# Performance work log

Measured on AMD Instinct MI355X. Metric: run time of the kernel, lower is better.

Reference implementation:

```python
import jax, jax.numpy as jnp
import numpy as np

B, N, C_IN, C_INTER = 32, 2048, 512, 512


def setup_inputs() -> dict:
    key = jax.random.key(0)
    ks = jax.random.split(key, 10)
    s_in = 1.0 / np.sqrt(C_IN)
    s_int = 1.0 / np.sqrt(C_INTER)
    return {
        "query": jax.random.normal(ks[0], (B, N, C_IN), jnp.float32),
        "key": jax.random.normal(ks[1], (B, N, C_IN), jnp.float32),
        "Wq": jax.random.normal(ks[2], (C_IN, C_INTER), jnp.float32) * s_in,
        "bq": jnp.zeros((C_INTER,), jnp.float32),
        "Wk": jax.random.normal(ks[3], (C_IN, C_INTER), jnp.float32) * s_in,
        "bk": jnp.zeros((C_INTER,), jnp.float32),
        "Wv": jax.random.normal(ks[4], (C_IN, C_INTER), jnp.float32) * s_in,
        "bv": jnp.zeros((C_INTER,), jnp.float32),
        "Wo": jax.random.normal(ks[5], (C_INTER, C_INTER), jnp.float32) * s_int,
        "bo": jnp.zeros((C_INTER,), jnp.float32),
    }


def reference(query, key, Wq, bq, Wk, bk, Wv, bv, Wo, bo):
    value = key  # value defaults to key in original forward
    q = jnp.einsum("bnc,cd->bnd", query, Wq) + bq   # [B,N,D]
    k = jnp.einsum("bnc,cd->bnd", key, Wk) + bk
    v = jnp.einsum("bnc,cd->bnd", value, Wv) + bv
    d = q.shape[-1]
    # non-standard scaling: divide by d (not sqrt(d))
    scores = jnp.einsum("bqd,bkd->bqk", q, k) / d    # [B,N,N]
    attn = jax.nn.softmax(scores, axis=-1)
    n_kv = attn.shape[-1]
    # second non-standard scaling: divide by number of keys
    out = jnp.einsum("bqk,bkd->bqd", attn, v) / n_kv
    return jnp.einsum("bnd,de->bne", out, Wo) + bo
```

## Files before the change

### kernel.cpp

```cpp
#include <hip/hip_runtime.h>
#include <stdint.h>

typedef unsigned short u16;
typedef __attribute__((ext_vector_type(8))) short bf16x8;
typedef __attribute__((ext_vector_type(4))) float f32x4;
typedef __attribute__((ext_vector_type(2))) unsigned int u32x2;
typedef __attribute__((ext_vector_type(4))) unsigned int u32x4;

__device__ __forceinline__ float bf2f(u16 u) {
  union { unsigned int i; float f; } v; v.i = ((unsigned int)u) << 16; return v.f;
}
__device__ __forceinline__ u16 f2bf(float f) {
  union { float f; unsigned int i; } v; v.f = f;
  unsigned int x = v.i;
  return (u16)((x + 0x7fffu + ((x >> 16) & 1u)) >> 16);
}

__device__ __forceinline__ void async16(const void* g, void* l) {
  __builtin_amdgcn_global_load_lds(
      (const __attribute__((address_space(1))) void*)g,
      (__attribute__((address_space(3))) void*)l, 16, 0, 0);
}

#define VMC6 asm volatile("s_waitcnt vmcnt(6)" ::: "memory")
#define VMC0 asm volatile("s_waitcnt vmcnt(0)" ::: "memory")
#define RAWBAR()                        \
  asm volatile("" ::: "memory");        \
  __builtin_amdgcn_s_barrier();         \
  asm volatile("" ::: "memory")

__global__ __launch_bounds__(256) void cast_f32_to_bf16(
    const float* __restrict__ x, u16* __restrict__ y, long n) {
  long i = ((long)blockIdx.x * blockDim.x + threadIdx.x) * 8;
  long stride = (long)gridDim.x * blockDim.x * 8;
  for (long j = i; j < n; j += stride) {
    float4 a = ((const float4*)(x + j))[0];
    float4 b = ((const float4*)(x + j))[1];
    u32x4 o;
    o.x = (unsigned)f2bf(a.x) | ((unsigned)f2bf(a.y) << 16);
    o.y = (unsigned)f2bf(a.z) | ((unsigned)f2bf(a.w) << 16);
    o.z = (unsigned)f2bf(b.x) | ((unsigned)f2bf(b.y) << 16);
    o.w = (unsigned)f2bf(b.z) | ((unsigned)f2bf(b.w) << 16);
    __builtin_nontemporal_store(o, (u32x4*)(y + j));
  }
}

__global__ __launch_bounds__(256) void castKT(
    const float* __restrict__ Kin, u16* __restrict__ Kb, u16* __restrict__ KbT) {
  __shared__ u16 tile[32][34];
  int t = threadIdx.x;
  long b = blockIdx.z;
  int n0 = blockIdx.x * 32, c0 = blockIdx.y * 32;
  int nr = t >> 3, c4 = (t & 7) * 4;
  float4 v = *(const float4*)(Kin + (b * 2048 + n0 + nr) * 512 + c0 + c4);
  unsigned q0 = f2bf(v.x), q1 = f2bf(v.y), q2 = f2bf(v.z), q3 = f2bf(v.w);
  u32x2 o1; o1.x = q0 | (q1 << 16); o1.y = q2 | (q3 << 16);
  __builtin_nontemporal_store(o1, (u32x2*)(Kb + (b * 2048 + n0 + nr) * 512 + c0 + c4));
  tile[nr][c4] = (u16)q0; tile[nr][c4 + 1] = (u16)q1;
  tile[nr][c4 + 2] = (u16)q2; tile[nr][c4 + 3] = (u16)q3;
  __syncthreads();
  int cr = t >> 3, n4 = (t & 7) * 4;
  unsigned r0 = tile[n4][cr], r1 = tile[n4 + 1][cr];
  unsigned r2 = tile[n4 + 2][cr], r3 = tile[n4 + 3][cr];
  u32x2 o2; o2.x = r0 | (r1 << 16); o2.y = r2 | (r3 << 16);
  __builtin_nontemporal_store(o2, (u32x2*)(KbT + (b * 512 + c0 + cr) * 2048 + n0 + n4));
}

__global__ __launch_bounds__(256) void smallGT(
    const float* __restrict__ Ai, const float* __restrict__ Bi, u16* __restrict__ C) {
  __shared__ float As[16][65], Bs[16][65];
  int t = threadIdx.x;
  int i0 = blockIdx.y * 16, j0 = blockIdx.x * 16;
  int r = t >> 4, c4 = (t & 15) * 4;
  int ty = t >> 4, tx = t & 15;
  float acc = 0.f;
  for (int d0 = 0; d0 < 512; d0 += 64) {
    float4 a = *(const float4*)(Ai + (i0 + r) * 512 + d0 + c4);
    float4 b = *(const float4*)(Bi + (j0 + r) * 512 + d0 + c4);
    __syncthreads();
    As[r][c4] = a.x; As[r][c4 + 1] = a.y; As[r][c4 + 2] = a.z; As[r][c4 + 3] = a.w;
    Bs[r][c4] = b.x; Bs[r][c4 + 1] = b.y; Bs[r][c4 + 2] = b.z; Bs[r][c4 + 3] = b.w;
    __syncthreads();
#pragma unroll
    for (int d = 0; d < 64; ++d) acc += As[ty][d] * Bs[tx][d];
  }
  C[(i0 + ty) * 512 + j0 + tx] = f2bf(acc);
}

__global__ __launch_bounds__(256) void smallW2T(
    const float* __restrict__ Wv, const float* __restrict__ Wo, u16* __restrict__ C) {
  __shared__ float Vs[16][65];
  __shared__ float Os[64][17];
  int t = threadIdx.x;
  int k0 = blockIdx.x * 16, n0 = blockIdx.y * 16;
  int r = t >> 4, c4 = (t & 15) * 4;
  int dd = t >> 2, nn4 = (t & 3) * 4;
  int ty = t >> 4, tx = t & 15;
  float acc = 0.f;
  for (int d0 = 0; d0 < 512; d0 += 64) {
    float4 a = *(const float4*)(Wv + (k0 + r) * 512 + d0 + c4);
    float4 b = *(const float4*)(Wo + (long)(d0 + dd) * 512 + n0 + nn4);
    __syncthreads();
    Vs[r][c4] = a.x; Vs[r][c4 + 1] = a.y; Vs[r][c4 + 2] = a.z; Vs[r][c4 + 3] = a.w;
    Os[dd][nn4] = b.x; Os[dd][nn4 + 1] = b.y; Os[dd][nn4 + 2] = b.z; Os[dd][nn4 + 3] = b.w;
    __syncthreads();
#pragma unroll
    for (int d = 0; d < 64; ++d) acc += Vs[tx][d] * Os[d][ty];
  }
  C[(n0 + ty) * 512 + k0 + tx] = f2bf(acc);
}

__global__ __launch_bounds__(256) void wveck(
    const float* __restrict__ Wk, const float* __restrict__ bq, float* __restrict__ wv) {
  int c = blockIdx.x, t = threadIdx.x;
  float s = 0.f;
  for (int d = t; d < 512; d += 256) s += Wk[c * 512 + d] * bq[d];
  for (int off = 32; off; off >>= 1) s += __shfl_xor(s, off);
  __shared__ float r4[4];
  if ((t & 63) == 0) r4[t >> 6] = s;
  __syncthreads();
  if (t == 0) wv[c] = (r4[0] + r4[1] + r4[2] + r4[3]) * (1.0f / 512.0f);
}

__global__ __launch_bounds__(256) void cveck(
    const float* __restrict__ Wo, const float* __restrict__ bv,
    const float* __restrict__ bo, float* __restrict__ c2) {
  int e = blockIdx.x * 256 + threadIdx.x;
  float s = 0.f;
  for (int d = 0; d < 512; ++d) s += bv[d] * Wo[d * 512 + e];
  c2[e] = s * (1.0f / 2048.0f) + bo[e];
}

__global__ __launch_bounds__(256) void betak(
    const u16* __restrict__ Kb, const float* __restrict__ wv, float* __restrict__ beta) {
  __shared__ float ws[512];
  int t = threadIdx.x, lane = t & 63, wid = t >> 6;
  ws[t] = wv[t];
  ws[t + 256] = wv[t + 256];
  __syncthreads();
  long row = (long)blockIdx.x * 4 + wid;
  bf16x8 v = *(const bf16x8*)(Kb + row * 512 + lane * 8);
  float s = 0.f;
#pragma unroll
  for (int j = 0; j < 8; ++j) s += bf2f((u16)v[j]) * ws[lane * 8 + j];
  for (int off = 32; off; off >>= 1) s += __shfl_xor(s, off);
  if (lane == 0) beta[row] = s;
}

__global__ __launch_bounds__(256) void rowred(
    const float* __restrict__ psum, float* __restrict__ rinv, int nrows) {
  int r = blockIdx.x * 256 + threadIdx.x;
  if (r >= nrows) return;
  const float* p = psum + (long)r * 32;
  float s = 0.f;
#pragma unroll
  for (int j = 0; j < 32; ++j) s += p[j];
  rinv[r] = 1.0f / s;
}

template <int MODE, int EXPO>
__global__ __launch_bounds__(256, 2) void gemm(
    const u16* __restrict__ A, const u16* __restrict__ B,
    const float* __restrict__ bias, long sBias,
    const float* __restrict__ rsc, float* __restrict__ psum,
    void* __restrict__ Cout,
    int N, int K, long sA, long sB, long sC, float scale,
    int mT, int nT, int Z, int nfast) {
  __shared__ __align__(16) char lds[3][24576];
  const int t = threadIdx.x;
  const int lane = t & 63;
  const int w = t >> 6;
  const int wm = w >> 1;
  const int wn = w & 1;

  const int wg = blockIdx.x;
  const int nb = mT * nT;
  long z; int within;
  if (Z > 1 && (Z & 7) == 0) {
    int xcd = wg & 7;
    int sub = wg >> 3;
    z = (long)(sub / nb) * 8 + xcd;
    within = sub % nb;
  } else {
    z = wg / nb;
    within = wg % nb;
  }
  int bx, by;
  if (nfast) { by = within % nT; bx = within / nT; }
  else       { bx = within % mT; by = within / mT; }
  const long m0 = (long)bx * 256;
  const int n0 = by * 128;
  const int nt = K >> 5;

  const int srow = w * 16 + (lane >> 2);
  const int koff = 8 * ((lane & 3) ^ ((lane >> 3) & 3));
  const u16* pa = A + z * sA + (m0 + srow) * (long)K + koff;
  const u16* pb = B + z * sB + ((long)(n0 + srow)) * K + koff;
  const int ldsW = w * 1024;

  const int fr = lane & 15;
  const int kb = (lane >> 4) * 16;
  const int sw = ((fr >> 1) & 3) << 4;
  const int aoff = (wm * 128 + fr) * 64 + (kb ^ sw);
  const int boff = 16384 + (wn * 64 + fr) * 64 + (kb ^ sw);

  f32x4 acc[8][4] = {};

#define STAGE(SLOT)                                                        \
  do {                                                                     \
    char* d_ = lds[SLOT] + ldsW;                                           \
    _Pragma("unroll") for (int c = 0; c < 4; ++c)                          \
        async16(pa + (long)c * 64 * K, d_ + c * 4096);                     \
    _Pragma("unroll") for (int c = 0; c < 2; ++c)                          \
        async16(pb + (long)c * 64 * K, d_ + 16384 + c * 4096);             \
    pa += 32; pb += 32;                                                    \
  } while (0)

  STAGE(0);
  STAGE(1);

  int slot = 0, stslot = 2;
  for (int tt = 0; tt < nt; ++tt) {
    if (tt < nt - 1) { VMC6; } else { VMC0; }
    RAWBAR();
    if (tt + 2 < nt) {
      STAGE(stslot);
      stslot = (stslot == 2) ? 0 : stslot + 1;
    }
    const char* rb = lds[slot];
    bf16x8 bf[4];
#pragma unroll
    for (int ni = 0; ni < 4; ++ni)
      bf[ni] = *(const bf16x8*)(rb + boff + ni * 1024);
    __builtin_amdgcn_s_setprio(1);
#pragma unroll
    for (int mi = 0; mi < 8; ++mi) {
      bf16x8 af = *(const bf16x8*)(rb + aoff + mi * 1024);
#pragma unroll
      for (int ni = 0; ni < 4; ++ni)
        acc[mi][ni] = __builtin_amdgcn_mfma_f32_16x16x32_bf16(af, bf[ni], acc[mi][ni], 0, 0, 0);
    }
    __builtin_amdgcn_s_setprio(0);
    slot = (slot == 2) ? 0 : slot + 1;
  }
#undef STAGE

  const int er = (lane >> 4) * 4;
  const int ec = lane & 15;
  float bvv[4];
#pragma unroll
  for (int ni = 0; ni < 4; ++ni)
    bvv[ni] = bias ? bias[z * sBias + n0 + wn * 64 + ni * 16 + ec] : 0.0f;
  if (MODE == 0) {
    u16* Ep = (u16*)lds;
    u16* Cp = (u16*)Cout + z * sC;
#pragma unroll
    for (int p = 0; p < 2; ++p) {
      __syncthreads();
      if (wm == p) {
#pragma unroll
        for (int mi = 0; mi < 8; ++mi) {
#pragma unroll
          for (int i = 0; i < 4; ++i) {
            int lrow = mi * 16 + er + i;
            float rv = 1.0f;
            if (!EXPO && rsc) rv = rsc[z * 2048 + m0 + wm * 128 + lrow];
            float rs = 0.f;
#pragma unroll
            for (int ni = 0; ni < 4; ++ni) {
              float val = acc[mi][ni][i] * scale + bvv[ni];
              if (EXPO) { val = __expf(val); rs += val; }
              else val *= rv;
              Ep[lrow * 136 + wn * 64 + ni * 16 + ec] = f2bf(val);
            }
            if (EXPO) {
              rs += __shfl_xor(rs, 1);
              rs += __shfl_xor(rs, 2);
              rs += __shfl_xor(rs, 4);
              rs += __shfl_xor(rs, 8);
              if (ec == 0)
                psum[((long)z * 2048 + m0 + wm * 128 + lrow) * 32 + by * 2 + wn] = rs;
            }
          }
        }
      }
      __syncthreads();
#pragma unroll
      for (int s = 0; s < 8; ++s) {
        int idx = s * 256 + t;
        int R = idx >> 4;
        int j = idx & 15;
        u32x4 d = *(const u32x4*)(Ep + R * 136 + j * 8);
        *(u32x4*)(Cp + (m0 + p * 128 + R) * (long)N + n0 + j * 8) = d;
      }
    }
  } else {
    float* Ep = (float*)lds;
    float* Cp = (float*)Cout + z * sC;
#pragma unroll
    for (int p = 0; p < 4; ++p) {
      __syncthreads();
      if (wm == (p >> 1)) {
#pragma unroll
        for (int mi2 = 0; mi2 < 4; ++mi2) {
          int mi = (p & 1) * 4 + mi2;
#pragma unroll
          for (int ni = 0; ni < 4; ++ni)
#pragma unroll
            for (int i = 0; i < 4; ++i)
              Ep[(mi2 * 16 + er + i) * 132 + wn * 64 + ni * 16 + ec] =
                  acc[mi][ni][i] * scale + bvv[ni];
        }
      }
      __syncthreads();
#pragma unroll
      for (int s = 0; s < 8; ++s) {
        int idx = s * 256 + t;
        int R = idx >> 5;
        int j = idx & 31;
        f32x4 d = *(const f32x4*)(Ep + R * 132 + j * 4);
        __builtin_nontemporal_store(
            d, (f32x4*)(Cp + (m0 + p * 64 + R) * (long)N + n0 + j * 4));
      }
    }
  }
}

extern "C" void kernel_launch(void* const* d_in, const int* in_sizes, int n_in,
                              void* d_out, int out_size, void* d_ws, size_t ws_size,
                              hipStream_t stream) {
  const float* query = (const float*)d_in[0];
  const float* key_  = (const float*)d_in[1];
  const float* Wq = (const float*)d_in[2];
  const float* bq = (const float*)d_in[3];
  const float* Wk = (const float*)d_in[4];
  const float* bk = (const float*)d_in[5];
  const float* Wv = (const float*)d_in[6];
  const float* bv = (const float*)d_in[7];
  const float* Wo = (const float*)d_in[8];
  const float* bo = (const float*)d_in[9];
  (void)bk;
  float* out = (float*)d_out;

  const long tokE = 65536L * 512;
  const long bstride = 2048L * 512;

  char* ws = (char*)d_ws;
  u16* Qb   = (u16*)(ws);
  u16* Kb   = (u16*)(ws + 67108864L);
  u16* KbT  = (u16*)(ws + 134217728L);
  u16* GT   = (u16*)(ws + 201326592L);
  u16* W2T  = (u16*)(ws + 201850880L);
  float* wv   = (float*)(ws + 202375168L);
  float* c2   = (float*)(ws + 202377216L);
  float* beta = (float*)(ws + 202379264L);
  float* rinv = (float*)(ws + 202641408L);
  char* Sbase = ws + 203423744L;
  u16* attn = Qb;

  u16* qb = (u16*)d_out;
  float* psum = (float*)((char*)d_out + 67108864L);

  long s_avail = (long)ws_size - 203423744L;
  int g = (int)(s_avail / 8388608L);
  if (g < 1) g = 1;
  if (g > 32) g = 32;
  if (g >= 8) g &= ~7;

  cast_f32_to_bf16<<<16384, 256, 0, stream>>>(query, Qb, tokE);
  castKT<<<dim3(64, 16, 32), 256, 0, stream>>>(key_, Kb, KbT);
  smallGT<<<dim3(32, 32), 256, 0, stream>>>(Wk, Wq, GT);
  smallW2T<<<dim3(32, 32), 256, 0, stream>>>(Wv, Wo, W2T);
  wveck<<<512, 256, 0, stream>>>(Wk, bq, wv);
  cveck<<<2, 256, 0, stream>>>(Wo, bv, bo, c2);
  betak<<<16384, 256, 0, stream>>>(Kb, wv, beta);

  gemm<0, 0><<<256 * 4, 256, 0, stream>>>(Qb, GT, nullptr, 0, nullptr, nullptr,
                                          qb, 512, 512, 0, 0, 0, 1.0f, 256, 4, 1, 0);

  for (int b0 = 0; b0 < 32; b0 += g) {
    int bc = (32 - b0 < g) ? (32 - b0) : g;
    u16* Sg = (u16*)Sbase;
    gemm<0, 1><<<8 * 16 * bc, 256, 0, stream>>>(
        qb + (long)b0 * bstride, Kb + (long)b0 * bstride,
        beta + (long)b0 * 2048, 2048, nullptr, psum, Sg, 2048, 512,
        bstride, bstride, 2048L * 2048, 1.0f / 512.0f, 8, 16, bc, 0);
    rowred<<<(bc * 2048 + 255) / 256, 256, 0, stream>>>(psum, rinv + b0 * 2048,
                                                        bc * 2048);
    gemm<0, 0><<<8 * 4 * bc, 256, 0, stream>>>(
        Sg, KbT + (long)b0 * bstride, nullptr, 0, rinv + b0 * 2048, nullptr,
        attn + (long)b0 * bstride, 512, 2048,
        2048L * 2048, bstride, bstride, 1.0f / 2048.0f, 8, 4, bc, 1);
  }

  gemm<2, 0><<<256 * 4, 256, 0, stream>>>(attn, W2T, c2, 0, nullptr, nullptr,
                                          out, 512, 512, 0, 0, 0, 1.0f, 256, 4, 1, 0);
}
```

Before: 736.5 us.

## Replace GEMM with 256x256-tile, 8-wave kernel using interleaved LDS ping-pong schedule

Replaces the 256x128-tile, 4-wave GEMM with a 256x256-tile, 512-thread kernel. It uses two 64-deep K buffers in 128KB LDS, explicit ds_read_b128 asm, and a hand-scheduled interleave of async global-to-LDS loads with MFMA blocks separated by barriers. This aims to raise arithmetic intensity per tile and to overlap loads with math across all four GEMM stages, with launch grids and psum indexing adjusted to match. The costs are fewer workgroups, heavy LDS use that limits occupancy, and many barriers per iteration.

```diff
diff --git a/kernel.cpp b/kernel.cpp
--- a/kernel.cpp
+++ b/kernel.cpp
@@ -22,12 +22,30 @@
       (__attribute__((address_space(3))) void*)l, 16, 0, 0);
 }
 
-#define VMC6 asm volatile("s_waitcnt vmcnt(6)" ::: "memory")
+#define VMC4 asm volatile("s_waitcnt vmcnt(4)" ::: "memory")
 #define VMC0 asm volatile("s_waitcnt vmcnt(0)" ::: "memory")
 #define RAWBAR()                        \
   asm volatile("" ::: "memory");        \
   __builtin_amdgcn_s_barrier();         \
   asm volatile("" ::: "memory")
+#define LGKM0                                             \
+  do {                                                    \
+    asm volatile("s_waitcnt lgkmcnt(0)" ::: "memory");    \
+    __builtin_amdgcn_sched_barrier(0);                    \
+  } while (0)
+
+#define DSR4(d, adr)                                                     \
+  asm volatile("ds_read_b128 %0, %4 offset:0\n\t"                        \
+               "ds_read_b128 %1, %4 offset:2048\n\t"                     \
+               "ds_read_b128 %2, %4 offset:4096\n\t"                     \
+               "ds_read_b128 %3, %4 offset:6144"                         \
+               : "=&v"(d[0]), "=&v"(d[1]), "=&v"(d[2]), "=&v"(d[3])      \
+               : "v"(adr))
+#define DSR2(d, adr)                                                     \
+  asm volatile("ds_read_b128 %0, %2 offset:0\n\t"                        \
+               "ds_read_b128 %1, %2 offset:2048"                         \
+               : "=&v"(d[0]), "=&v"(d[1])                                \
+               : "v"(adr))
 
 __global__ __launch_bounds__(256) void cast_f32_to_bf16(
     const float* __restrict__ x, u16* __restrict__ y, long n) {
@@ -159,91 +177,138 @@
 }
 
 template <int MODE, int EXPO>
-__global__ __launch_bounds__(256, 2) void gemm(
+__global__ __launch_bounds__(512, 2) void gemm256(
     const u16* __restrict__ A, const u16* __restrict__ B,
     const float* __restrict__ bias, long sBias,
     const float* __restrict__ rsc, float* __restrict__ psum,
     void* __restrict__ Cout,
     int N, int K, long sA, long sB, long sC, float scale,
     int mT, int nT, int Z, int nfast) {
-  __shared__ __align__(16) char lds[3][24576];
+  __shared__ __align__(16) char lds[131072];
   const int t = threadIdx.x;
   const int lane = t & 63;
   const int w = t >> 6;
-  const int wm = w >> 1;
-  const int wn = w & 1;
+  const int wm = w >> 2;
+  const int wn = w & 3;
 
   const int wg = blockIdx.x;
   const int nb = mT * nT;
   long z; int within;
   if (Z > 1 && (Z & 7) == 0) {
-    int xcd = wg & 7;
-    int sub = wg >> 3;
+    int xcd = wg & 7, sub = wg >> 3;
     z = (long)(sub / nb) * 8 + xcd;
     within = sub % nb;
-  } else {
-    z = wg / nb;
-    within = wg % nb;
-  }
+  } else { z = wg / nb; within = wg % nb; }
   int bx, by;
   if (nfast) { by = within % nT; bx = within / nT; }
   else       { bx = within % mT; by = within / mT; }
   const long m0 = (long)bx * 256;
-  const int n0 = by * 128;
-  const int nt = K >> 5;
-
-  const int srow = w * 16 + (lane >> 2);
-  const int koff = 8 * ((lane & 3) ^ ((lane >> 3) & 3));
-  const u16* pa = A + z * sA + (m0 + srow) * (long)K + koff;
-  const u16* pb = B + z * sB + ((long)(n0 + srow)) * K + koff;
-  const int ldsW = w * 1024;
+  const int n0 = by * 256;
+  const int nt = K >> 6;
+  const int niter = nt >> 1;
+
+  const int srow = t >> 3;
+  const int sslot = (t & 7) ^ (srow & 7);
+  const u16* pa = A + z * sA + (m0 + srow) * (long)K + sslot * 8;
+  const u16* pb = B + z * sB + (n0 + srow) * (long)K + sslot * 8;
+  const int sdst = t * 16;
 
   const int fr = lane & 15;
-  const int kb = (lane >> 4) * 16;
-  const int sw = ((fr >> 1) & 3) << 4;
-  const int aoff = (wm * 128 + fr) * 64 + (kb ^ sw);
-  const int boff = 16384 + (wn * 64 + fr) * 64 + (kb ^ sw);
-
+  const int hi4 = lane >> 4;
+  const int s7 = fr & 7;
+  const unsigned ldsb =
+      (unsigned)(uintptr_t)(__attribute__((address_space(3))) char*)lds;
+  const unsigned kc0 = (unsigned)(((hi4) ^ s7) * 16);
+  const unsigned kc1 = (unsigned)(((4 + hi4) ^ s7) * 16);
+  const unsigned arow = ldsb + (wm * 128 + fr) * 128;
+  const unsigned brow = ldsb + 32768 + (wn * 64 + fr) * 128;
+
+  bf16x8 a[2][4], b0[2][2], b1[2][2];
   f32x4 acc[8][4] = {};
 
-#define STAGE(SLOT)                                                        \
-  do {                                                                     \
-    char* d_ = lds[SLOT] + ldsW;                                           \
-    _Pragma("unroll") for (int c = 0; c < 4; ++c)                          \
-        async16(pa + (long)c * 64 * K, d_ + c * 4096);                     \
-    _Pragma("unroll") for (int c = 0; c < 2; ++c)                          \
-        async16(pb + (long)c * 64 * K, d_ + 16384 + c * 4096);             \
-    pa += 32; pb += 32;                                                    \
+#define STG_A(BUF, H, KT)                                        \
+  do {                                                           \
+    char* d_ = (char*)lds + (BUF) + (H) * 16384 + sdst;          \
+    const u16* g_ = pa + (long)(KT) * 64 + (long)(H) * 128 * K;  \
+    async16(g_, d_);                                             \
+    async16(g_ + 64L * K, d_ + 8192);                            \
   } while (0)
-
-  STAGE(0);
-  STAGE(1);
-
-  int slot = 0, stslot = 2;
-  for (int tt = 0; tt < nt; ++tt) {
-    if (tt < nt - 1) { VMC6; } else { VMC0; }
-    RAWBAR();
-    if (tt + 2 < nt) {
-      STAGE(stslot);
-      stslot = (stslot == 2) ? 0 : stslot + 1;
-    }
-    const char* rb = lds[slot];
-    bf16x8 bf[4];
-#pragma unroll
-    for (int ni = 0; ni < 4; ++ni)
-      bf[ni] = *(const bf16x8*)(rb + boff + ni * 1024);
-    __builtin_amdgcn_s_setprio(1);
-#pragma unroll
-    for (int mi = 0; mi < 8; ++mi) {
-      bf16x8 af = *(const bf16x8*)(rb + aoff + mi * 1024);
-#pragma unroll
-      for (int ni = 0; ni < 4; ++ni)
-        acc[mi][ni] = __builtin_amdgcn_mfma_f32_16x16x32_bf16(af, bf[ni], acc[mi][ni], 0, 0, 0);
-    }
-    __builtin_amdgcn_s_setprio(0);
-    slot = (slot == 2) ? 0 : slot + 1;
-  }
-#undef STAGE
+#define STG_B(BUF, H, KT)                                        \
+  do {                                                           \
+    char* d_ = (char*)lds + (BUF) + 32768 + (H) * 16384 + sdst;  \
+    const u16* g_ = pb + (long)(KT) * 64 + (long)(H) * 128 * K;  \
+    async16(g_, d_);                                             \
+    async16(g_ + 64L * K, d_ + 8192);                            \
+  } while (0)
+#define RD_A0(BUF) do { DSR4(a[0], arow + (BUF) + kc0); DSR4(a[1], arow + (BUF) + kc1); } while (0)
+#define RD_A1(BUF) do { DSR4(a[0], arow + (BUF) + 8192 + kc0); DSR4(a[1], arow + (BUF) + 8192 + kc1); } while (0)
+#define RD_B0(BUF) do { DSR2(b0[0], brow + (BUF) + kc0); DSR2(b0[1], brow + (BUF) + kc1); } while (0)
+#define RD_B1(BUF) do { DSR2(b1[0], brow + (BUF) + 4096 + kc0); DSR2(b1[1], brow + (BUF) + 4096 + kc1); } while (0)
+#define MF(Rb, Cb, Bs)                                                        \
+  do {                                                                        \
+    __builtin_amdgcn_s_setprio(1);                                            \
+    _Pragma("unroll") for (int kk = 0; kk < 2; ++kk)                          \
+    _Pragma("unroll") for (int mi = 0; mi < 4; ++mi)                          \
+    _Pragma("unroll") for (int ni = 0; ni < 2; ++ni)                          \
+        acc[(Rb) + mi][(Cb) + ni] = __builtin_amdgcn_mfma_f32_16x16x32_bf16(  \
+            a[kk][mi], Bs[kk][ni], acc[(Rb) + mi][(Cb) + ni], 0, 0, 0);       \
+    __builtin_amdgcn_s_setprio(0);                                            \
+  } while (0)
+
+  STG_A(0, 0, 0); STG_A(0, 1, 0); STG_B(0, 0, 0); STG_B(0, 1, 0);
+  STG_B(65536, 0, 1); STG_B(65536, 1, 1);
+  VMC4;
+  RAWBAR();
+
+  for (int it = 0; it < niter; ++it) {
+    const int T = it * 2;
+    const bool more = (it + 1 < niter);
+    RD_A0(0); RD_B0(0);
+    STG_A(65536, 0, T + 1);
+    RAWBAR(); LGKM0;
+    MF(0, 0, b0);
+    RAWBAR();
+    RD_B1(0);
+    STG_A(65536, 1, T + 1);
+    RAWBAR(); LGKM0;
+    MF(0, 2, b1);
+    RAWBAR();
+    RD_A1(0);
+    if (more) STG_B(0, 0, T + 2);
+    RAWBAR(); LGKM0;
+    MF(4, 2, b1);
+    RAWBAR();
+    if (more) { STG_B(0, 1, T + 2); VMC4; } else { VMC0; }
+    RAWBAR();
+    MF(4, 0, b0);
+    RAWBAR();
+    RD_A0(65536); RD_B0(65536);
+    if (more) STG_A(0, 0, T + 2);
+    RAWBAR(); LGKM0;
+    MF(0, 0, b0);
+    RAWBAR();
+    RD_B1(65536);
+    if (more) STG_A(0, 1, T + 2);
+    RAWBAR(); LGKM0;
+    MF(0, 2, b1);
+    RAWBAR();
+    RD_A1(65536);
+    if (more) STG_B(65536, 0, T + 3);
+    RAWBAR(); LGKM0;
+    MF(4, 2, b1);
+    RAWBAR();
+    if (more) { STG_B(65536, 1, T + 3); VMC4; }
+    RAWBAR();
+    MF(4, 0, b0);
+    RAWBAR();
+  }
+#undef STG_A
+#undef STG_B
+#undef RD_A0
+#undef RD_A1
+#undef RD_B0
+#undef RD_B1
+#undef MF
 
   const int er = (lane >> 4) * 4;
   const int ec = lane & 15;
@@ -271,7 +336,7 @@
               float val = acc[mi][ni][i] * scale + bvv[ni];
               if (EXPO) { val = __expf(val); rs += val; }
               else val *= rv;
-              Ep[lrow * 136 + wn * 64 + ni * 16 + ec] = f2bf(val);
+              Ep[lrow * 264 + wn * 64 + ni * 16 + ec] = f2bf(val);
             }
             if (EXPO) {
               rs += __shfl_xor(rs, 1);
@@ -279,7 +344,7 @@
               rs += __shfl_xor(rs, 4);
               rs += __shfl_xor(rs, 8);
               if (ec == 0)
-                psum[((long)z * 2048 + m0 + wm * 128 + lrow) * 32 + by * 2 + wn] = rs;
+                psum[((long)z * 2048 + m0 + wm * 128 + lrow) * 32 + by * 4 + wn] = rs;
             }
           }
         }
@@ -287,11 +352,12 @@
       __syncthreads();
 #pragma unroll
       for (int s = 0; s < 8; ++s) {
-        int idx = s * 256 + t;
-        int R = idx >> 4;
-        int j = idx & 15;
-        u32x4 d = *(const u32x4*)(Ep + R * 136 + j * 8);
-        *(u32x4*)(Cp + (m0 + p * 128 + R) * (long)N + n0 + j * 8) = d;
+        int idx = s * 512 + t;
+        int R = idx >> 5;
+        int j = idx & 31;
+        u32x4 d = *(const u32x4*)(Ep + R * 264 + j * 8);
+        __builtin_nontemporal_store(
+            d, (u32x4*)(Cp + (m0 + p * 128 + R) * (long)N + n0 + j * 8));
       }
     }
   } else {
@@ -308,17 +374,17 @@
           for (int ni = 0; ni < 4; ++ni)
 #pragma unroll
             for (int i = 0; i < 4; ++i)
-              Ep[(mi2 * 16 + er + i) * 132 + wn * 64 + ni * 16 + ec] =
+              Ep[(mi2 * 16 + er + i) * 264 + wn * 64 + ni * 16 + ec] =
                   acc[mi][ni][i] * scale + bvv[ni];
         }
       }
       __syncthreads();
 #pragma unroll
       for (int s = 0; s < 8; ++s) {
-        int idx = s * 256 + t;
-        int R = idx >> 5;
-        int j = idx & 31;
-        f32x4 d = *(const f32x4*)(Ep + R * 132 + j * 4);
+        int idx = s * 512 + t;
+        int R = idx >> 6;
+        int j = idx & 63;
+        f32x4 d = *(const f32x4*)(Ep + R * 264 + j * 4);
         __builtin_nontemporal_store(
             d, (f32x4*)(Cp + (m0 + p * 64 + R) * (long)N + n0 + j * 4));
       }
@@ -375,24 +441,24 @@
   cveck<<<2, 256, 0, stream>>>(Wo, bv, bo, c2);
   betak<<<16384, 256, 0, stream>>>(Kb, wv, beta);
 
-  gemm<0, 0><<<256 * 4, 256, 0, stream>>>(Qb, GT, nullptr, 0, nullptr, nullptr,
-                                          qb, 512, 512, 0, 0, 0, 1.0f, 256, 4, 1, 0);
+  gemm256<0, 0><<<512, 512, 0, stream>>>(Qb, GT, nullptr, 0, nullptr, nullptr,
+                                         qb, 512, 512, 0, 0, 0, 1.0f, 256, 2, 1, 0);
 
   for (int b0 = 0; b0 < 32; b0 += g) {
     int bc = (32 - b0 < g) ? (32 - b0) : g;
     u16* Sg = (u16*)Sbase;
-    gemm<0, 1><<<8 * 16 * bc, 256, 0, stream>>>(
+    gemm256<0, 1><<<8 * 8 * bc, 512, 0, stream>>>(
         qb + (long)b0 * bstride, Kb + (long)b0 * bstride,
         beta + (long)b0 * 2048, 2048, nullptr, psum, Sg, 2048, 512,
-        bstride, bstride, 2048L * 2048, 1.0f / 512.0f, 8, 16, bc, 0);
+        bstride, bstride, 2048L * 2048, 1.0f / 512.0f, 8, 8, bc, 0);
     rowred<<<(bc * 2048 + 255) / 256, 256, 0, stream>>>(psum, rinv + b0 * 2048,
                                                         bc * 2048);
-    gemm<0, 0><<<8 * 4 * bc, 256, 0, stream>>>(
+    gemm256<0, 0><<<8 * 2 * bc, 512, 0, stream>>>(
         Sg, KbT + (long)b0 * bstride, nullptr, 0, rinv + b0 * 2048, nullptr,
         attn + (long)b0 * bstride, 512, 2048,
-        2048L * 2048, bstride, bstride, 1.0f / 2048.0f, 8, 4, bc, 1);
-  }
-
-  gemm<2, 0><<<256 * 4, 256, 0, stream>>>(attn, W2T, c2, 0, nullptr, nullptr,
-                                          out, 512, 512, 0, 0, 0, 1.0f, 256, 4, 1, 0);
-}
+        2048L * 2048, bstride, bstride, 1.0f / 2048.0f, 8, 2, bc, 1);
+  }
+
+  gemm256<2, 0><<<512, 512, 0, stream>>>(attn, W2T, c2, 0, nullptr, nullptr,
+                                         out, 512, 512, 0, 0, 0, 1.0f, 256, 2, 1, 0);
+}
```

After: 678.8 us. -7.8%, faster.

## Fuse query fp32-to-bf16 cast into projection GEMM and switch to double buffering

Applied to the files above, without the earlier changes.

Removes the standalone query cast kernel. The first GEMM now reads fp32 query rows directly, converts them to bf16 in registers and writes them swizzled into LDS. The GEMM main loop changes from a 3-slot async pipeline with vmcnt waits to a 2-slot double buffer with __syncthreads, which shrinks LDS so launch bounds can allow 3 blocks per CU. Non-score outputs now use nontemporal stores. This saves a full read and write pass over the query tensor, but the shallower pipeline and per-iteration barriers may expose more memory latency in every GEMM.

```diff
diff --git a/kernel.cpp b/kernel.cpp
--- a/kernel.cpp
+++ b/kernel.cpp
@@ -20,29 +20,6 @@
   __builtin_amdgcn_global_load_lds(
       (const __attribute__((address_space(1))) void*)g,
       (__attribute__((address_space(3))) void*)l, 16, 0, 0);
-}
-
-#define VMC6 asm volatile("s_waitcnt vmcnt(6)" ::: "memory")
-#define VMC0 asm volatile("s_waitcnt vmcnt(0)" ::: "memory")
-#define RAWBAR()                        \
-  asm volatile("" ::: "memory");        \
-  __builtin_amdgcn_s_barrier();         \
-  asm volatile("" ::: "memory")
-
-__global__ __launch_bounds__(256) void cast_f32_to_bf16(
-    const float* __restrict__ x, u16* __restrict__ y, long n) {
-  long i = ((long)blockIdx.x * blockDim.x + threadIdx.x) * 8;
-  long stride = (long)gridDim.x * blockDim.x * 8;
-  for (long j = i; j < n; j += stride) {
-    float4 a = ((const float4*)(x + j))[0];
-    float4 b = ((const float4*)(x + j))[1];
-    u32x4 o;
-    o.x = (unsigned)f2bf(a.x) | ((unsigned)f2bf(a.y) << 16);
-    o.y = (unsigned)f2bf(a.z) | ((unsigned)f2bf(a.w) << 16);
-    o.z = (unsigned)f2bf(b.x) | ((unsigned)f2bf(b.y) << 16);
-    o.w = (unsigned)f2bf(b.z) | ((unsigned)f2bf(b.w) << 16);
-    __builtin_nontemporal_store(o, (u32x4*)(y + j));
-  }
 }
 
 __global__ __launch_bounds__(256) void castKT(
@@ -158,15 +135,15 @@
   rinv[r] = 1.0f / s;
 }
 
-template <int MODE, int EXPO>
-__global__ __launch_bounds__(256, 2) void gemm(
-    const u16* __restrict__ A, const u16* __restrict__ B,
+template <int MODE, int EXPO, int FA>
+__global__ __launch_bounds__(256, 3) void gemm(
+    const void* __restrict__ Ain, const u16* __restrict__ B,
     const float* __restrict__ bias, long sBias,
     const float* __restrict__ rsc, float* __restrict__ psum,
     void* __restrict__ Cout,
     int N, int K, long sA, long sB, long sC, float scale,
     int mT, int nT, int Z, int nfast) {
-  __shared__ __align__(16) char lds[3][24576];
+  __shared__ __align__(16) char lds[2][24576];
   const int t = threadIdx.x;
   const int lane = t & 63;
   const int w = t >> 6;
@@ -177,14 +154,10 @@
   const int nb = mT * nT;
   long z; int within;
   if (Z > 1 && (Z & 7) == 0) {
-    int xcd = wg & 7;
-    int sub = wg >> 3;
+    int xcd = wg & 7, sub = wg >> 3;
     z = (long)(sub / nb) * 8 + xcd;
     within = sub % nb;
-  } else {
-    z = wg / nb;
-    within = wg % nb;
-  }
+  } else { z = wg / nb; within = wg % nb; }
   int bx, by;
   if (nfast) { by = within % nT; bx = within / nT; }
   else       { bx = within % mT; by = within / mT; }
@@ -194,9 +167,14 @@
 
   const int srow = w * 16 + (lane >> 2);
   const int koff = 8 * ((lane & 3) ^ ((lane >> 3) & 3));
-  const u16* pa = A + z * sA + (m0 + srow) * (long)K + koff;
+  const u16* pa = (const u16*)Ain + z * sA + (m0 + srow) * (long)K + koff;
   const u16* pb = B + z * sB + ((long)(n0 + srow)) * K + koff;
   const int ldsW = w * 1024;
+
+  const float* paf = nullptr;
+  const int swzt = ((t >> 1) & 3) << 4;
+  if (FA) paf = (const float*)Ain + (m0 + t) * (long)K;
+  float4 fv[8];
 
   const int fr = lane & 15;
   const int kb = (lane >> 4) * 16;
@@ -206,28 +184,44 @@
 
   f32x4 acc[8][4] = {};
 
-#define STAGE(SLOT)                                                        \
+#define LOAD_AF(KT)                                                        \
+  _Pragma("unroll") for (int j = 0; j < 8; ++j)                            \
+      fv[j] = *(const float4*)(paf + (KT) * 32 + j * 4)
+#define WRITE_AF(BUF)                                                      \
+  _Pragma("unroll") for (int c = 0; c < 4; ++c) {                          \
+    u32x4 o_;                                                              \
+    o_.x = (unsigned)f2bf(fv[2 * c].x) | ((unsigned)f2bf(fv[2 * c].y) << 16); \
+    o_.y = (unsigned)f2bf(fv[2 * c].z) | ((unsigned)f2bf(fv[2 * c].w) << 16); \
+    o_.z = (unsigned)f2bf(fv[2 * c + 1].x) | ((unsigned)f2bf(fv[2 * c + 1].y) << 16); \
+    o_.w = (unsigned)f2bf(fv[2 * c + 1].z) | ((unsigned)f2bf(fv[2 * c + 1].w) << 16); \
+    *(u32x4*)(lds[BUF] + t * 64 + ((c * 16) ^ swzt)) = o_;                 \
+  }
+#define STAGE_A16(BUF)                                                     \
   do {                                                                     \
-    char* d_ = lds[SLOT] + ldsW;                                           \
+    char* d_ = lds[BUF] + ldsW;                                            \
     _Pragma("unroll") for (int c = 0; c < 4; ++c)                          \
         async16(pa + (long)c * 64 * K, d_ + c * 4096);                     \
+    pa += 32;                                                              \
+  } while (0)
+#define STAGE_B16(BUF)                                                     \
+  do {                                                                     \
+    char* d_ = lds[BUF] + 16384 + ldsW;                                    \
     _Pragma("unroll") for (int c = 0; c < 2; ++c)                          \
-        async16(pb + (long)c * 64 * K, d_ + 16384 + c * 4096);             \
-    pa += 32; pb += 32;                                                    \
+        async16(pb + (long)c * 64 * K, d_ + c * 4096);                     \
+    pb += 32;                                                              \
   } while (0)
 
-  STAGE(0);
-  STAGE(1);
-
-  int slot = 0, stslot = 2;
+  if (FA) { LOAD_AF(0); WRITE_AF(0); } else { STAGE_A16(0); }
+  STAGE_B16(0);
+  __syncthreads();
+
+  int cur = 0;
   for (int tt = 0; tt < nt; ++tt) {
-    if (tt < nt - 1) { VMC6; } else { VMC0; }
-    RAWBAR();
-    if (tt + 2 < nt) {
-      STAGE(stslot);
-      stslot = (stslot == 2) ? 0 : stslot + 1;
+    if (tt + 1 < nt) {
+      if (FA) { LOAD_AF(tt + 1); } else { STAGE_A16(cur ^ 1); }
+      STAGE_B16(cur ^ 1);
     }
-    const char* rb = lds[slot];
+    const char* rb = lds[cur];
     bf16x8 bf[4];
 #pragma unroll
     for (int ni = 0; ni < 4; ++ni)
@@ -241,9 +235,14 @@
         acc[mi][ni] = __builtin_amdgcn_mfma_f32_16x16x32_bf16(af, bf[ni], acc[mi][ni], 0, 0, 0);
     }
     __builtin_amdgcn_s_setprio(0);
-    slot = (slot == 2) ? 0 : slot + 1;
-  }
-#undef STAGE
+    if (FA && tt + 1 < nt) { WRITE_AF(cur ^ 1); }
+    __syncthreads();
+    cur ^= 1;
+  }
+#undef LOAD_AF
+#undef WRITE_AF
+#undef STAGE_A16
+#undef STAGE_B16
 
   const int er = (lane >> 4) * 4;
   const int ec = lane & 15;
@@ -291,7 +290,9 @@
         int R = idx >> 4;
         int j = idx & 15;
         u32x4 d = *(const u32x4*)(Ep + R * 136 + j * 8);
-        *(u32x4*)(Cp + (m0 + p * 128 + R) * (long)N + n0 + j * 8) = d;
+        u32x4* dst = (u32x4*)(Cp + (m0 + p * 128 + R) * (long)N + n0 + j * 8);
+        if (EXPO) *dst = d;
+        else __builtin_nontemporal_store(d, dst);
       }
     }
   } else {
@@ -342,11 +343,9 @@
   (void)bk;
   float* out = (float*)d_out;
 
-  const long tokE = 65536L * 512;
   const long bstride = 2048L * 512;
 
   char* ws = (char*)d_ws;
-  u16* Qb   = (u16*)(ws);
   u16* Kb   = (u16*)(ws + 67108864L);
   u16* KbT  = (u16*)(ws + 134217728L);
   u16* GT   = (u16*)(ws + 201326592L);
@@ -356,7 +355,7 @@
   float* beta = (float*)(ws + 202379264L);
   float* rinv = (float*)(ws + 202641408L);
   char* Sbase = ws + 203423744L;
-  u16* attn = Qb;
+  u16* attn = (u16*)ws;
 
   u16* qb = (u16*)d_out;
   float* psum = (float*)((char*)d_out + 67108864L);
@@ -367,7 +366,6 @@
   if (g > 32) g = 32;
   if (g >= 8) g &= ~7;
 
-  cast_f32_to_bf16<<<16384, 256, 0, stream>>>(query, Qb, tokE);
   castKT<<<dim3(64, 16, 32), 256, 0, stream>>>(key_, Kb, KbT);
   smallGT<<<dim3(32, 32), 256, 0, stream>>>(Wk, Wq, GT);
   smallW2T<<<dim3(32, 32), 256, 0, stream>>>(Wv, Wo, W2T);
@@ -375,24 +373,25 @@
   cveck<<<2, 256, 0, stream>>>(Wo, bv, bo, c2);
   betak<<<16384, 256, 0, stream>>>(Kb, wv, beta);
 
-  gemm<0, 0><<<256 * 4, 256, 0, stream>>>(Qb, GT, nullptr, 0, nullptr, nullptr,
-                                          qb, 512, 512, 0, 0, 0, 1.0f, 256, 4, 1, 0);
+  gemm<0, 0, 1><<<256 * 4, 256, 0, stream>>>(
+      query, GT, nullptr, 0, nullptr, nullptr, qb,
+      512, 512, 0, 0, 0, 1.0f, 256, 4, 1, 0);
 
   for (int b0 = 0; b0 < 32; b0 += g) {
     int bc = (32 - b0 < g) ? (32 - b0) : g;
     u16* Sg = (u16*)Sbase;
-    gemm<0, 1><<<8 * 16 * bc, 256, 0, stream>>>(
+    gemm<0, 1, 0><<<8 * 16 * bc, 256, 0, stream>>>(
         qb + (long)b0 * bstride, Kb + (long)b0 * bstride,
         beta + (long)b0 * 2048, 2048, nullptr, psum, Sg, 2048, 512,
         bstride, bstride, 2048L * 2048, 1.0f / 512.0f, 8, 16, bc, 0);
-    rowred<<<(bc * 2048 + 255) / 256, 256, 0, stream>>>(psum, rinv + b0 * 2048,
-                                                        bc * 2048);
-    gemm<0, 0><<<8 * 4 * bc, 256, 0, stream>>>(
-        Sg, KbT + (long)b0 * bstride, nullptr, 0, rinv + b0 * 2048, nullptr,
+    rowred<<<(bc * 2048 + 255) / 256, 256, 0, stream>>>(psum, rinv, bc * 2048);
+    gemm<0, 0, 0><<<8 * 4 * bc, 256, 0, stream>>>(
+        Sg, KbT + (long)b0 * bstride, nullptr, 0, rinv, nullptr,
         attn + (long)b0 * bstride, 512, 2048,
         2048L * 2048, bstride, bstride, 1.0f / 2048.0f, 8, 4, bc, 1);
   }
 
-  gemm<2, 0><<<256 * 4, 256, 0, stream>>>(attn, W2T, c2, 0, nullptr, nullptr,
-                                          out, 512, 512, 0, 0, 0, 1.0f, 256, 4, 1, 0);
-}
+  gemm<2, 0, 0><<<256 * 4, 256, 0, stream>>>(
+      attn, W2T, c2, 0, nullptr, nullptr, out,
+      512, 512, 0, 0, 0, 1.0f, 256, 4, 1, 0);
+}
```

After: 1.129 ms. 53.4% more time.

## Switch GEMM to double-buffered LDS with syncthreads, raise occupancy to three blocks

Applied to the files above, without the earlier changes.

Replaces the triple-buffered LDS pipeline, which relied on explicit vmcnt waits and raw barriers, with a simpler double buffer synchronized by __syncthreads. This cuts LDS per block from 72KB to 48KB, and launch bounds now target three blocks per CU. Non-EXPO bf16 output stores become nontemporal. The rinv pointer is no longer offset per batch chunk, so the buffer is reused across chunks. The trade is a shallower prefetch that may expose load latency, with a full barrier every k-step. The loop also no longer appears to wait on the async LDS loads before reading, which risks a read-before-arrival race.

```diff
diff --git a/kernel.cpp b/kernel.cpp
--- a/kernel.cpp
+++ b/kernel.cpp
@@ -21,13 +21,6 @@
       (const __attribute__((address_space(1))) void*)g,
       (__attribute__((address_space(3))) void*)l, 16, 0, 0);
 }
-
-#define VMC6 asm volatile("s_waitcnt vmcnt(6)" ::: "memory")
-#define VMC0 asm volatile("s_waitcnt vmcnt(0)" ::: "memory")
-#define RAWBAR()                        \
-  asm volatile("" ::: "memory");        \
-  __builtin_amdgcn_s_barrier();         \
-  asm volatile("" ::: "memory")
 
 __global__ __launch_bounds__(256) void cast_f32_to_bf16(
     const float* __restrict__ x, u16* __restrict__ y, long n) {
@@ -159,14 +152,14 @@
 }
 
 template <int MODE, int EXPO>
-__global__ __launch_bounds__(256, 2) void gemm(
+__global__ __launch_bounds__(256, 3) void gemm(
     const u16* __restrict__ A, const u16* __restrict__ B,
     const float* __restrict__ bias, long sBias,
     const float* __restrict__ rsc, float* __restrict__ psum,
     void* __restrict__ Cout,
     int N, int K, long sA, long sB, long sC, float scale,
     int mT, int nT, int Z, int nfast) {
-  __shared__ __align__(16) char lds[3][24576];
+  __shared__ __align__(16) char lds[2][24576];
   const int t = threadIdx.x;
   const int lane = t & 63;
   const int w = t >> 6;
@@ -177,14 +170,10 @@
   const int nb = mT * nT;
   long z; int within;
   if (Z > 1 && (Z & 7) == 0) {
-    int xcd = wg & 7;
-    int sub = wg >> 3;
+    int xcd = wg & 7, sub = wg >> 3;
     z = (long)(sub / nb) * 8 + xcd;
     within = sub % nb;
-  } else {
-    z = wg / nb;
-    within = wg % nb;
-  }
+  } else { z = wg / nb; within = wg % nb; }
   int bx, by;
   if (nfast) { by = within % nT; bx = within / nT; }
   else       { bx = within % mT; by = within / mT; }
@@ -206,9 +195,9 @@
 
   f32x4 acc[8][4] = {};
 
-#define STAGE(SLOT)                                                        \
+#define STAGE(BUF)                                                         \
   do {                                                                     \
-    char* d_ = lds[SLOT] + ldsW;                                           \
+    char* d_ = lds[BUF] + ldsW;                                            \
     _Pragma("unroll") for (int c = 0; c < 4; ++c)                          \
         async16(pa + (long)c * 64 * K, d_ + c * 4096);                     \
     _Pragma("unroll") for (int c = 0; c < 2; ++c)                          \
@@ -217,17 +206,12 @@
   } while (0)
 
   STAGE(0);
-  STAGE(1);
-
-  int slot = 0, stslot = 2;
+  __syncthreads();
+
+  int cur = 0;
   for (int tt = 0; tt < nt; ++tt) {
-    if (tt < nt - 1) { VMC6; } else { VMC0; }
-    RAWBAR();
-    if (tt + 2 < nt) {
-      STAGE(stslot);
-      stslot = (stslot == 2) ? 0 : stslot + 1;
-    }
-    const char* rb = lds[slot];
+    if (tt + 1 < nt) STAGE(cur ^ 1);
+    const char* rb = lds[cur];
     bf16x8 bf[4];
 #pragma unroll
     for (int ni = 0; ni < 4; ++ni)
@@ -241,7 +225,8 @@
         acc[mi][ni] = __builtin_amdgcn_mfma_f32_16x16x32_bf16(af, bf[ni], acc[mi][ni], 0, 0, 0);
     }
     __builtin_amdgcn_s_setprio(0);
-    slot = (slot == 2) ? 0 : slot + 1;
+    __syncthreads();
+    cur ^= 1;
   }
 #undef STAGE
 
@@ -291,7 +276,9 @@
         int R = idx >> 4;
         int j = idx & 15;
         u32x4 d = *(const u32x4*)(Ep + R * 136 + j * 8);
-        *(u32x4*)(Cp + (m0 + p * 128 + R) * (long)N + n0 + j * 8) = d;
+        u32x4* dst = (u32x4*)(Cp + (m0 + p * 128 + R) * (long)N + n0 + j * 8);
+        if (EXPO) *dst = d;
+        else __builtin_nontemporal_store(d, dst);
       }
     }
   } else {
@@ -375,8 +362,9 @@
   cveck<<<2, 256, 0, stream>>>(Wo, bv, bo, c2);
   betak<<<16384, 256, 0, stream>>>(Kb, wv, beta);
 
-  gemm<0, 0><<<256 * 4, 256, 0, stream>>>(Qb, GT, nullptr, 0, nullptr, nullptr,
-                                          qb, 512, 512, 0, 0, 0, 1.0f, 256, 4, 1, 0);
+  gemm<0, 0><<<256 * 4, 256, 0, stream>>>(
+      Qb, GT, nullptr, 0, nullptr, nullptr, qb,
+      512, 512, 0, 0, 0, 1.0f, 256, 4, 1, 0);
 
   for (int b0 = 0; b0 < 32; b0 += g) {
     int bc = (32 - b0 < g) ? (32 - b0) : g;
@@ -385,14 +373,14 @@
         qb + (long)b0 * bstride, Kb + (long)b0 * bstride,
         beta + (long)b0 * 2048, 2048, nullptr, psum, Sg, 2048, 512,
         bstride, bstride, 2048L * 2048, 1.0f / 512.0f, 8, 16, bc, 0);
-    rowred<<<(bc * 2048 + 255) / 256, 256, 0, stream>>>(psum, rinv + b0 * 2048,
-                                                        bc * 2048);
+    rowred<<<(bc * 2048 + 255) / 256, 256, 0, stream>>>(psum, rinv, bc * 2048);
     gemm<0, 0><<<8 * 4 * bc, 256, 0, stream>>>(
-        Sg, KbT + (long)b0 * bstride, nullptr, 0, rinv + b0 * 2048, nullptr,
+        Sg, KbT + (long)b0 * bstride, nullptr, 0, rinv, nullptr,
         attn + (long)b0 * bstride, 512, 2048,
         2048L * 2048, bstride, bstride, 1.0f / 2048.0f, 8, 4, bc, 1);
   }
 
-  gemm<2, 0><<<256 * 4, 256, 0, stream>>>(attn, W2T, c2, 0, nullptr, nullptr,
-                                          out, 512, 512, 0, 0, 0, 1.0f, 256, 4, 1, 0);
-}
+  gemm<2, 0><<<256 * 4, 256, 0, stream>>>(
+      attn, W2T, c2, 0, nullptr, nullptr, out,
+      512, 512, 0, 0, 0, 1.0f, 256, 4, 1, 0);
+}
```

Result: faster. 713.0 us (-3.2%).
